# Kernel optimization log

Hardware: AMD Instinct MI355X
Metric: run time of the kernel (lower is better)

Reference implementation:

```python
import jax, jax.numpy as jnp
import numpy as np


def _build_skew(coeff, gate, left, right):
    # coeff: [B, r], gate: [B], left/right: [F, r]
    scaled_left = left[None, :, :] * coeff[:, None, :]          # [B, F, r]
    base = jnp.einsum('bfr,gr->bfg', scaled_left, right)         # [B, F, F]
    skew = base - jnp.swapaxes(base, -1, -2)
    return gate[:, None, None] * skew


def setup_inputs() -> dict:
    key = jax.random.key(0)
    ks = jax.random.split(key, 10)
    B, N, F, R = 8, 4096, 512, 16
    return {
        'x': jax.random.normal(ks[0], (B, N, F), dtype=jnp.float32),
        'coeff': jax.random.normal(ks[1], (B, R), dtype=jnp.float32),
        'gate': jax.random.uniform(ks[2], (B,), dtype=jnp.float32),
        'coeff_local': jax.random.normal(ks[3], (B, R), dtype=jnp.float32),
        'gate_local': jax.random.uniform(ks[4], (B,), dtype=jnp.float32),
        'comm_scale': jax.random.uniform(ks[5], (B,), dtype=jnp.float32),
        'left': jax.random.normal(ks[6], (F, R), dtype=jnp.float32) / np.sqrt(F),
        'right': jax.random.normal(ks[7], (F, R), dtype=jnp.float32) / np.sqrt(F),
        'left_local': jax.random.normal(ks[8], (F, R), dtype=jnp.float32) / np.sqrt(F),
        'right_local': jax.random.normal(ks[9], (F, R), dtype=jnp.float32) / np.sqrt(F),
    }


def reference(x, coeff, gate, coeff_local, gate_local, comm_scale,
              left, right, left_local, right_local):
    F_dim = left.shape[0]
    global_skew = _build_skew(coeff, gate, left, right)                  # [B, F, F]
    local_skew = _build_skew(coeff_local, gate_local, left_local, right_local)
    omega = 0.5 * (global_skew + local_skew)
    commutator = local_skew @ global_skew - global_skew @ local_skew
    omega = omega + comm_scale[:, None, None] * (commutator / 12.0)
    eye = jnp.eye(F_dim, dtype=jnp.float32)[None, :, :]
    # Cayley transform: (I - 0.5*Omega)^{-1} (I + 0.5*Omega)
    transform = jnp.linalg.solve(eye - 0.5 * omega, eye + 0.5 * omega)   # [B, F, F]
    mixed = jnp.einsum('bnd,bdh->bnh', x, transform)
    return mixed.astype(x.dtype)
```

## Files before the change

kernel.cpp:

```cpp
#include <hip/hip_runtime.h>

#define B_ 8
#define N_ 4096
#define F_ 512

typedef __attribute__((ext_vector_type(8))) short bf16x8;
typedef __attribute__((ext_vector_type(4))) float f32x4;

__device__ __forceinline__ float Sval(const float* l, const float* r,
                                      const float* ll, const float* rl,
                                      int h, int e) {
    const int m = e >> 4, c = e & 15;
    const float* p = (m == 0) ? l : (m == 1) ? r : (m == 2) ? ll : rl;
    return p[h * 16 + c];
}

__device__ __forceinline__ float qval(const float* coeff, const float* coeff_l,
                                      int b, int j) {
    if (j < 16) return 1.f;
    if (j < 32) return coeff[b * 16 + (j - 16)];
    if (j < 48) return 1.f;
    return coeff_l[b * 16 + (j - 48)];
}

__device__ __forceinline__ float lane_bcast(float v, int lane) {
    return __int_as_float(__builtin_amdgcn_readlane(__float_as_int(v), lane));
}

__device__ __forceinline__ unsigned short bf16_rn(float x) {
    unsigned u = __float_as_uint(x);
    unsigned r = u + 0x7FFFu + ((u >> 16) & 1u);
    return (unsigned short)(r >> 16);
}

__device__ __forceinline__ void bf16_split(float x, short& hi, short& lo) {
    const unsigned short h = bf16_rn(x);
    const float hf = __uint_as_float(((unsigned)h) << 16);
    const unsigned short s = bf16_rn(x - hf);
    hi = (short)h; lo = (short)s;
}

__global__ __launch_bounds__(256) void k_prep(const float* l, const float* r,
                                              const float* ll, const float* rl,
                                              float* GS, unsigned short* Sf) {
    __shared__ float red[4][64];
    const int i = blockIdx.x;
    const int t = threadIdx.x;
    const int j = t & 63, seg = t >> 6;

    {
        const int ht = i >> 1, eh = i & 1;
        for (int idx = t; idx < 512; idx += 256) {
            const int lx = idx >> 3, ii = idx & 7;
            const int h = ht * 16 + (lx & 15);
            const int e = eh * 32 + ((lx >> 4) & 3) * 8 + ii;
            short hh, ss;
            bf16_split(Sval(l, r, ll, rl, h, e), hh, ss);
            Sf[(i * 2 + 0) * 512 + idx] = (unsigned short)hh;
            Sf[(i * 2 + 1) * 512 + idx] = (unsigned short)ss;
        }
    }

    float acc = 0.f;
    const int h0 = seg * 128;
    for (int h = h0; h < h0 + 128; ++h)
        acc += Sval(l, r, ll, rl, h, i) * Sval(l, r, ll, rl, h, j);
    red[seg][j] = acc;
    __syncthreads();
    if (t < 64) GS[i * 64 + t] = red[0][t] + red[1][t] + red[2][t] + red[3][t];
}

#define DO64(M, K) \
    M(0, K) M(1, K) M(2, K) M(3, K) M(4, K) M(5, K) M(6, K) M(7, K) \
    M(8, K) M(9, K) M(10, K) M(11, K) M(12, K) M(13, K) M(14, K) M(15, K) \
    M(16, K) M(17, K) M(18, K) M(19, K) M(20, K) M(21, K) M(22, K) M(23, K) \
    M(24, K) M(25, K) M(26, K) M(27, K) M(28, K) M(29, K) M(30, K) M(31, K) \
    M(32, K) M(33, K) M(34, K) M(35, K) M(36, K) M(37, K) M(38, K) M(39, K) \
    M(40, K) M(41, K) M(42, K) M(43, K) M(44, K) M(45, K) M(46, K) M(47, K) \
    M(48, K) M(49, K) M(50, K) M(51, K) M(52, K) M(53, K) M(54, K) M(55, K) \
    M(56, K) M(57, K) M(58, K) M(59, K) M(60, K) M(61, K) M(62, K) M(63, K)

#define GJ_LOAD(RR, K) a[RR] = MsL[(RR) * 64 + t];
#define GJ_STORE(RR, K) KsL[(RR) * 64 + t] = a[RR];
#define GJ_UPD(RR, K) \
    if ((RR) != (K)) { \
        const float f = lane_bcast(a[RR], (K)); \
        a[RR] = ((t == (K)) ? 0.f : a[RR]) - f * a[K]; \
    }
#define GJ_STEP(K) { \
    const float dk = lane_bcast(a[K], (K)); \
    const float pinv = 1.0f / dk; \
    a[K] = (t == (K)) ? pinv : a[K] * pinv; \
    DO64(GJ_UPD, K) \
}

__global__ __launch_bounds__(256, 1) void k_solve(const float* coeff, const float* gate,
                                                  const float* coeff_l, const float* gate_l,
                                                  const float* comm, const float* GS,
                                                  float* Eout) {
    __shared__ float smem[16384];
    float* CPs = smem;
    float* GST = smem + 4096;
    float* MsL = smem + 8192;
    float* KsL = smem + 12288;
    float* ABs = MsL;
    float* u1s = KsL;
    float* u2s = KsL + 32;

    const int b = blockIdx.x, t = threadIdx.x;
    const int tx = t & 15, ty = t >> 4;
    const float g = gate[b], gl = gate_l[b];
    const float cs = comm[b] / 12.0f;

    if (t < 32) {
        u1s[t] = (t < 16) ? g * coeff[b * 16 + t] : -g;
        u2s[t] = (t < 16) ? gl * coeff_l[b * 16 + t] : -gl;
    }
    for (int idx = t; idx < 4096; idx += 256) {
        const int i = idx & 63, e = idx >> 6;
        GST[idx] = -0.5f * qval(coeff, coeff_l, b, i) * GS[(i ^ 16) * 64 + e];
    }
    __syncthreads();

    for (int idx = t; idx < 2048; idx += 256) {
        const int which = idx >> 10;
        const int i = (idx >> 5) & 31, j = idx & 31;
        float val;
        if (which == 0) {
            const int v2i = (i < 16) ? 48 + i : 16 + i;
            const float v2sc = (i < 16) ? 1.f : coeff_l[b * 16 + (i - 16)];
            val = v2sc * u1s[j] * GS[v2i * 64 + j];
        } else {
            const int v1i = (i < 16) ? 16 + i : i - 16;
            const float v1sc = (i < 16) ? 1.f : coeff[b * 16 + (i - 16)];
            val = v1sc * u2s[j] * GS[v1i * 64 + 32 + j];
        }
        ABs[idx] = val;
    }
    __syncthreads();

    for (int idx = t; idx < 4096; idx += 256) {
        const int e = idx >> 6, j = idx & 63;
        float val = 0.f;
        if (j < 32) {
            if (e == j) val += 0.5f * u1s[j];
            if (e >= 32) val += cs * u2s[e - 32] * ABs[(e - 32) * 32 + j];
        } else {
            const int jp = j - 32;
            if (e == 32 + jp) val += 0.5f * u2s[jp];
            if (e < 32) val -= cs * u1s[e] * ABs[1024 + e * 32 + jp];
        }
        CPs[idx] = val;
    }
    __syncthreads();

    {
        const int i0 = ty * 4, m0 = tx * 4;
        float acc[4][4];
#pragma unroll
        for (int i = 0; i < 4; ++i)
#pragma unroll
            for (int j = 0; j < 4; ++j) acc[i][j] = 0.f;
        for (int e = 0; e < 64; ++e) {
            const float4 av = *reinterpret_cast<const float4*>(&GST[e * 64 + i0]);
            const float4 bv = *reinterpret_cast<const float4*>(&CPs[e * 64 + m0]);
            const float a[4] = {av.x, av.y, av.z, av.w};
            const float bb[4] = {bv.x, bv.y, bv.z, bv.w};
#pragma unroll
            for (int i = 0; i < 4; ++i)
#pragma unroll
                for (int j = 0; j < 4; ++j) acc[i][j] += a[i] * bb[j];
        }
        __syncthreads();
#pragma unroll
        for (int i = 0; i < 4; ++i)
#pragma unroll
            for (int j = 0; j < 4; ++j)
                MsL[(i0 + i) * 64 + m0 + j] =
                    acc[i][j] + (((i0 + i) == (m0 + j)) ? 1.f : 0.f);
    }
    __syncthreads();

    if (t < 64) {
        float a[64];
        DO64(GJ_LOAD, 0)
        GJ_STEP(0) GJ_STEP(1) GJ_STEP(2) GJ_STEP(3)
        GJ_STEP(4) GJ_STEP(5) GJ_STEP(6) GJ_STEP(7)
        GJ_STEP(8) GJ_STEP(9) GJ_STEP(10) GJ_STEP(11)
        GJ_STEP(12) GJ_STEP(13) GJ_STEP(14) GJ_STEP(15)
        GJ_STEP(16) GJ_STEP(17) GJ_STEP(18) GJ_STEP(19)
        GJ_STEP(20) GJ_STEP(21) GJ_STEP(22) GJ_STEP(23)
        GJ_STEP(24) GJ_STEP(25) GJ_STEP(26) GJ_STEP(27)
        GJ_STEP(28) GJ_STEP(29) GJ_STEP(30) GJ_STEP(31)
        GJ_STEP(32) GJ_STEP(33) GJ_STEP(34) GJ_STEP(35)
        GJ_STEP(36) GJ_STEP(37) GJ_STEP(38) GJ_STEP(39)
        GJ_STEP(40) GJ_STEP(41) GJ_STEP(42) GJ_STEP(43)
        GJ_STEP(44) GJ_STEP(45) GJ_STEP(46) GJ_STEP(47)
        GJ_STEP(48) GJ_STEP(49) GJ_STEP(50) GJ_STEP(51)
        GJ_STEP(52) GJ_STEP(53) GJ_STEP(54) GJ_STEP(55)
        GJ_STEP(56) GJ_STEP(57) GJ_STEP(58) GJ_STEP(59)
        GJ_STEP(60) GJ_STEP(61) GJ_STEP(62) GJ_STEP(63)
        DO64(GJ_STORE, 0)
    }
    __syncthreads();

    {
        const int i0 = ty * 4, j0 = tx * 4;
        float accd[4][4], acca[4][4];
#pragma unroll
        for (int i = 0; i < 4; ++i)
#pragma unroll
            for (int j = 0; j < 4; ++j) { accd[i][j] = 0.f; acca[i][j] = 0.f; }
        for (int q = 0; q < 64; ++q) {
            const float4 bv = *reinterpret_cast<const float4*>(&KsL[q * 64 + j0]);
            const float bb[4] = {bv.x, bv.y, bv.z, bv.w};
            float ad[4], aa[4];
#pragma unroll
            for (int i = 0; i < 4; ++i) {
                ad[i] = CPs[(i0 + i) * 64 + q];
                aa[i] = MsL[(i0 + i) * 64 + q];
            }
#pragma unroll
            for (int i = 0; i < 4; ++i)
#pragma unroll
                for (int j = 0; j < 4; ++j) {
                    accd[i][j] += ad[i] * bb[j];
                    acca[i][j] += aa[i] * bb[j];
                }
        }
        __syncthreads();
#pragma unroll
        for (int i = 0; i < 4; ++i)
#pragma unroll
            for (int j = 0; j < 4; ++j) {
                GST[(i0 + i) * 64 + j0 + j] = accd[i][j];
                CPs[(i0 + i) * 64 + j0 + j] = acca[i][j];
            }
    }
    __syncthreads();

    {
        const int e0 = ty * 4, c0 = tx * 4;
        float acc[4][4];
#pragma unroll
        for (int i = 0; i < 4; ++i)
#pragma unroll
            for (int j = 0; j < 4; ++j) acc[i][j] = 0.f;
        for (int q = 0; q < 64; ++q) {
            const float4 bv = *reinterpret_cast<const float4*>(&CPs[q * 64 + c0]);
            const float bb[4] = {bv.x, bv.y, bv.z, bv.w};
            float a[4];
#pragma unroll
            for (int i = 0; i < 4; ++i) a[i] = GST[(e0 + i) * 64 + q];
#pragma unroll
            for (int i = 0; i < 4; ++i)
#pragma unroll
                for (int j = 0; j < 4; ++j) acc[i][j] += a[i] * bb[j];
        }
        float qv[4];
#pragma unroll
        for (int j = 0; j < 4; ++j) qv[j] = qval(coeff, coeff_l, b, c0 + j);
#pragma unroll
        for (int i = 0; i < 4; ++i) {
            float4 o;
            o.x = qv[0] * (2.f * GST[(e0 + i) * 64 + c0 + 0] - acc[i][0]);
            o.y = qv[1] * (2.f * GST[(e0 + i) * 64 + c0 + 1] - acc[i][1]);
            o.z = qv[2] * (2.f * GST[(e0 + i) * 64 + c0 + 2] - acc[i][2]);
            o.w = qv[3] * (2.f * GST[(e0 + i) * 64 + c0 + 3] - acc[i][3]);
            *reinterpret_cast<float4*>(&Eout[b * 4096 + (e0 + i) * 64 + (c0 ^ 16)]) = o;
        }
    }
}

__global__ __launch_bounds__(256) void k_se(const float* l, const float* r,
                                            const float* ll, const float* rl,
                                            const float* Ein, unsigned short* SEf) {
    __shared__ float Es[4096];
    __shared__ float Ss[64 * 66];
    __shared__ float SEs[64 * 65];
    const int b = blockIdx.y, hc = blockIdx.x, t = threadIdx.x;
    for (int idx = t; idx < 4096; idx += 256) {
        Es[idx] = Ein[b * 4096 + idx];
        const int hl_ = idx >> 6, e = idx & 63;
        Ss[hl_ * 66 + e] = Sval(l, r, ll, rl, hc * 64 + hl_, e);
    }
    __syncthreads();

    const int h = t >> 2;
    const int mg = (t & 3) * 16;
    float acc[16];
#pragma unroll
    for (int q = 0; q < 16; ++q) acc[q] = 0.f;
#pragma unroll 4
    for (int e = 0; e < 64; ++e) {
        const float s = Ss[h * 66 + e];
        const float* Er = Es + e * 64 + mg;
#pragma unroll
        for (int q = 0; q < 16; ++q) acc[q] += s * Er[q];
    }
#pragma unroll
    for (int q = 0; q < 16; ++q) SEs[h * 65 + mg + q] = acc[q];
    __syncthreads();

    unsigned short* outp = SEf + (size_t)b * 65536 + hc * 8192;
#pragma unroll
    for (int it = 0; it < 4; ++it) {
        const int widx0 = it * 2048 + t * 8;
        const int fl = widx0 >> 10;
        const int hl = (widx0 >> 9) & 1;
        const int lx = (widx0 >> 3) & 63;
        const int m = (fl & 3) * 16 + (lx & 15);
        const int hb = (fl >> 2) * 32 + ((lx >> 4) & 3) * 8;
        unsigned short wv[8];
#pragma unroll
        for (int i = 0; i < 8; ++i) {
            short hh, ss;
            bf16_split(SEs[(hb + i) * 65 + m], hh, ss);
            wv[i] = hl ? (unsigned short)ss : (unsigned short)hh;
        }
        uint4 pk;
        pk.x = (unsigned)wv[0] | ((unsigned)wv[1] << 16);
        pk.y = (unsigned)wv[2] | ((unsigned)wv[3] << 16);
        pk.z = (unsigned)wv[4] | ((unsigned)wv[5] << 16);
        pk.w = (unsigned)wv[6] | ((unsigned)wv[7] << 16);
        *reinterpret_cast<uint4*>(outp + widx0) = pk;
    }
}

__global__ __launch_bounds__(256, 4) void k_mix(const float* x,
                                                const unsigned short* SEf,
                                                const unsigned short* Sf,
                                                float* out) {
    __shared__ float Zs[32 * 68];
    const int b = blockIdx.y;
    const int r0 = blockIdx.x * 32;
    const int t = threadIdx.x;
    const int w = t >> 6;
    const int l = t & 63;
    const int lm = l & 15;
    const int lk = (l >> 4) * 8;
    const int rw = w & 1, cw = w >> 1;
    const float* xb = x + (size_t)b * N_ * F_;
    float* outb = out + (size_t)b * N_ * F_;
    const unsigned short* sef = SEf + (size_t)b * 65536;

    f32x4 ahh0 = {0.f, 0.f, 0.f, 0.f}, alh0 = ahh0, ahl0 = ahh0;
    f32x4 ahh1 = ahh0, alh1 = ahh0, ahl1 = ahh0;
    const int arow = r0 + 16 * rw + lm;
    const float* xrow = xb + (size_t)arow * F_;
#pragma unroll 2
    for (int kk = 0; kk < 16; ++kk) {
        const int k0 = kk * 32 + lk;
        const float4 xa = *reinterpret_cast<const float4*>(xrow + k0);
        const float4 xc = *reinterpret_cast<const float4*>(xrow + k0 + 4);
        const float xs[8] = {xa.x, xa.y, xa.z, xa.w, xc.x, xc.y, xc.z, xc.w};
        bf16x8 ah, al;
#pragma unroll
        for (int i = 0; i < 8; ++i) {
            short hh, ss;
            bf16_split(xs[i], hh, ss);
            ah[i] = hh; al[i] = ss;
        }
        const int o0 = (kk * 4 + 2 * cw) * 1024 + l * 8;
        const bf16x8 bh0 = *reinterpret_cast<const bf16x8*>(sef + o0);
        const bf16x8 bl0 = *reinterpret_cast<const bf16x8*>(sef + o0 + 512);
        const bf16x8 bh1 = *reinterpret_cast<const bf16x8*>(sef + o0 + 1024);
        const bf16x8 bl1 = *reinterpret_cast<const bf16x8*>(sef + o0 + 1536);
        ahh0 = __builtin_amdgcn_mfma_f32_16x16x32_bf16(ah, bh0, ahh0, 0, 0, 0);
        alh0 = __builtin_amdgcn_mfma_f32_16x16x32_bf16(al, bh0, alh0, 0, 0, 0);
        ahl0 = __builtin_amdgcn_mfma_f32_16x16x32_bf16(ah, bl0, ahl0, 0, 0, 0);
        ahh1 = __builtin_amdgcn_mfma_f32_16x16x32_bf16(ah, bh1, ahh1, 0, 0, 0);
        alh1 = __builtin_amdgcn_mfma_f32_16x16x32_bf16(al, bh1, alh1, 0, 0, 0);
        ahl1 = __builtin_amdgcn_mfma_f32_16x16x32_bf16(ah, bl1, ahl1, 0, 0, 0);
    }
#pragma unroll
    for (int r = 0; r < 4; ++r) {
        const int zr = (16 * rw + (l >> 4) * 4 + r) * 68 + 32 * cw;
        Zs[zr + lm] = ahh0[r] + alh0[r] + ahl0[r];
        Zs[zr + 16 + lm] = ahh1[r] + alh1[r] + ahl1[r];
    }
    __syncthreads();

    bf16x8 zh0, zl0, zh1, zl1;
    {
        const float* zrow = &Zs[(16 * rw + lm) * 68];
#pragma unroll
        for (int i = 0; i < 8; ++i) {
            short hh, ss;
            bf16_split(zrow[lk + i], hh, ss);
            zh0[i] = hh; zl0[i] = ss;
            bf16_split(zrow[32 + lk + i], hh, ss);
            zh1[i] = hh; zl1[i] = ss;
        }
    }
    const int orow0 = r0 + 16 * rw + (l >> 4) * 4;
#pragma unroll 2
    for (int j2 = 0; j2 < 16; ++j2) {
        const int ht = cw * 16 + j2;
        const int h0 = ht * 16 + lm;
        f32x4 ca = {0.f, 0.f, 0.f, 0.f};
        f32x4 cb;
#pragma unroll
        for (int r = 0; r < 4; ++r) cb[r] = xb[(size_t)(orow0 + r) * F_ + h0];
        const int fb = ht * 2048 + l * 8;
        const bf16x8 bh0 = *reinterpret_cast<const bf16x8*>(Sf + fb);
        const bf16x8 bl0 = *reinterpret_cast<const bf16x8*>(Sf + fb + 512);
        const bf16x8 bh1 = *reinterpret_cast<const bf16x8*>(Sf + fb + 1024);
        const bf16x8 bl1 = *reinterpret_cast<const bf16x8*>(Sf + fb + 1536);
        ca = __builtin_amdgcn_mfma_f32_16x16x32_bf16(zh0, bh0, ca, 0, 0, 0);
        ca = __builtin_amdgcn_mfma_f32_16x16x32_bf16(zl0, bh0, ca, 0, 0, 0);
        ca = __builtin_amdgcn_mfma_f32_16x16x32_bf16(zh0, bl0, ca, 0, 0, 0);
        cb = __builtin_amdgcn_mfma_f32_16x16x32_bf16(zh1, bh1, cb, 0, 0, 0);
        cb = __builtin_amdgcn_mfma_f32_16x16x32_bf16(zl1, bh1, cb, 0, 0, 0);
        cb = __builtin_amdgcn_mfma_f32_16x16x32_bf16(zh1, bl1, cb, 0, 0, 0);
#pragma unroll
        for (int r = 0; r < 4; ++r)
            outb[(size_t)(orow0 + r) * F_ + h0] = ca[r] + cb[r];
    }
}

extern "C" void kernel_launch(void* const* d_in, const int* in_sizes, int n_in,
                              void* d_out, int out_size, void* d_ws, size_t ws_size,
                              hipStream_t stream) {
    (void)in_sizes; (void)n_in; (void)out_size; (void)ws_size;
    const float* x       = (const float*)d_in[0];
    const float* coeff   = (const float*)d_in[1];
    const float* gate    = (const float*)d_in[2];
    const float* coeff_l = (const float*)d_in[3];
    const float* gate_l  = (const float*)d_in[4];
    const float* comm    = (const float*)d_in[5];
    const float* l       = (const float*)d_in[6];
    const float* r       = (const float*)d_in[7];
    const float* ll      = (const float*)d_in[8];
    const float* rl      = (const float*)d_in[9];

    char* wsb = (char*)d_ws;
    float* GS = (float*)(wsb);
    float* E  = (float*)(wsb + 16384);
    unsigned short* SEf = (unsigned short*)(wsb + 147456);
    unsigned short* Sf  = (unsigned short*)(wsb + 1196032);
    float* out = (float*)d_out;

    k_prep<<<dim3(64), dim3(256), 0, stream>>>(l, r, ll, rl, GS, Sf);
    k_solve<<<dim3(8), dim3(256), 0, stream>>>(coeff, gate, coeff_l, gate_l, comm, GS, E);
    k_se<<<dim3(8, 8), dim3(256), 0, stream>>>(l, r, ll, rl, E, SEf);
    k_mix<<<dim3(128, 8), dim3(256), 0, stream>>>(x, SEf, Sf, out);
}
```

Baseline: 123.7 us.

## Split small-matrix solve kernel into pre, Gauss-Jordan inverse, and post kernels

The fused k_solve kernel is split into three launches. k_pre builds M and CP and writes them to workspace. k_inv runs the 64x64 register-resident Gauss-Jordan inverse in a 64-thread block, and k_post does the trailing matmuls. This separates the register-heavy inverse from the 256-thread shared-memory matmul phases, which may improve register allocation and remove idle threads during the inverse. The cost is two extra launches and global-memory round trips for M, CP and K on a tiny 8-block serial path.

```diff
diff --git a/kernel.cpp b/kernel.cpp
--- a/kernel.cpp
+++ b/kernel.cpp
@@ -70,42 +70,14 @@
     if (t < 64) GS[i * 64 + t] = red[0][t] + red[1][t] + red[2][t] + red[3][t];
 }
 
-#define DO64(M, K) \
-    M(0, K) M(1, K) M(2, K) M(3, K) M(4, K) M(5, K) M(6, K) M(7, K) \
-    M(8, K) M(9, K) M(10, K) M(11, K) M(12, K) M(13, K) M(14, K) M(15, K) \
-    M(16, K) M(17, K) M(18, K) M(19, K) M(20, K) M(21, K) M(22, K) M(23, K) \
-    M(24, K) M(25, K) M(26, K) M(27, K) M(28, K) M(29, K) M(30, K) M(31, K) \
-    M(32, K) M(33, K) M(34, K) M(35, K) M(36, K) M(37, K) M(38, K) M(39, K) \
-    M(40, K) M(41, K) M(42, K) M(43, K) M(44, K) M(45, K) M(46, K) M(47, K) \
-    M(48, K) M(49, K) M(50, K) M(51, K) M(52, K) M(53, K) M(54, K) M(55, K) \
-    M(56, K) M(57, K) M(58, K) M(59, K) M(60, K) M(61, K) M(62, K) M(63, K)
-
-#define GJ_LOAD(RR, K) a[RR] = MsL[(RR) * 64 + t];
-#define GJ_STORE(RR, K) KsL[(RR) * 64 + t] = a[RR];
-#define GJ_UPD(RR, K) \
-    if ((RR) != (K)) { \
-        const float f = lane_bcast(a[RR], (K)); \
-        a[RR] = ((t == (K)) ? 0.f : a[RR]) - f * a[K]; \
-    }
-#define GJ_STEP(K) { \
-    const float dk = lane_bcast(a[K], (K)); \
-    const float pinv = 1.0f / dk; \
-    a[K] = (t == (K)) ? pinv : a[K] * pinv; \
-    DO64(GJ_UPD, K) \
-}
-
-__global__ __launch_bounds__(256, 1) void k_solve(const float* coeff, const float* gate,
-                                                  const float* coeff_l, const float* gate_l,
-                                                  const float* comm, const float* GS,
-                                                  float* Eout) {
-    __shared__ float smem[16384];
-    float* CPs = smem;
-    float* GST = smem + 4096;
-    float* MsL = smem + 8192;
-    float* KsL = smem + 12288;
-    float* ABs = MsL;
-    float* u1s = KsL;
-    float* u2s = KsL + 32;
+__global__ __launch_bounds__(256) void k_pre(const float* coeff, const float* gate,
+                                             const float* coeff_l, const float* gate_l,
+                                             const float* comm, const float* GS,
+                                             float* Mws, float* CPws) {
+    __shared__ float GST[4096];
+    __shared__ float CPs[4096];
+    __shared__ float ABs[2048];
+    __shared__ float u1s[32], u2s[32];
 
     const int b = blockIdx.x, t = threadIdx.x;
     const int tx = t & 15, ty = t >> 4;
@@ -151,6 +123,7 @@
             if (e < 32) val -= cs * u1s[e] * ABs[1024 + e * 32 + jp];
         }
         CPs[idx] = val;
+        CPws[b * 4096 + idx] = val;
     }
     __syncthreads();
 
@@ -171,36 +144,77 @@
 #pragma unroll
                 for (int j = 0; j < 4; ++j) acc[i][j] += a[i] * bb[j];
         }
-        __syncthreads();
-#pragma unroll
-        for (int i = 0; i < 4; ++i)
-#pragma unroll
-            for (int j = 0; j < 4; ++j)
-                MsL[(i0 + i) * 64 + m0 + j] =
-                    acc[i][j] + (((i0 + i) == (m0 + j)) ? 1.f : 0.f);
-    }
-    __syncthreads();
-
-    if (t < 64) {
-        float a[64];
-        DO64(GJ_LOAD, 0)
-        GJ_STEP(0) GJ_STEP(1) GJ_STEP(2) GJ_STEP(3)
-        GJ_STEP(4) GJ_STEP(5) GJ_STEP(6) GJ_STEP(7)
-        GJ_STEP(8) GJ_STEP(9) GJ_STEP(10) GJ_STEP(11)
-        GJ_STEP(12) GJ_STEP(13) GJ_STEP(14) GJ_STEP(15)
-        GJ_STEP(16) GJ_STEP(17) GJ_STEP(18) GJ_STEP(19)
-        GJ_STEP(20) GJ_STEP(21) GJ_STEP(22) GJ_STEP(23)
-        GJ_STEP(24) GJ_STEP(25) GJ_STEP(26) GJ_STEP(27)
-        GJ_STEP(28) GJ_STEP(29) GJ_STEP(30) GJ_STEP(31)
-        GJ_STEP(32) GJ_STEP(33) GJ_STEP(34) GJ_STEP(35)
-        GJ_STEP(36) GJ_STEP(37) GJ_STEP(38) GJ_STEP(39)
-        GJ_STEP(40) GJ_STEP(41) GJ_STEP(42) GJ_STEP(43)
-        GJ_STEP(44) GJ_STEP(45) GJ_STEP(46) GJ_STEP(47)
-        GJ_STEP(48) GJ_STEP(49) GJ_STEP(50) GJ_STEP(51)
-        GJ_STEP(52) GJ_STEP(53) GJ_STEP(54) GJ_STEP(55)
-        GJ_STEP(56) GJ_STEP(57) GJ_STEP(58) GJ_STEP(59)
-        GJ_STEP(60) GJ_STEP(61) GJ_STEP(62) GJ_STEP(63)
-        DO64(GJ_STORE, 0)
+#pragma unroll
+        for (int i = 0; i < 4; ++i) {
+            float4 o;
+            o.x = acc[i][0] + (((i0 + i) == (m0 + 0)) ? 1.f : 0.f);
+            o.y = acc[i][1] + (((i0 + i) == (m0 + 1)) ? 1.f : 0.f);
+            o.z = acc[i][2] + (((i0 + i) == (m0 + 2)) ? 1.f : 0.f);
+            o.w = acc[i][3] + (((i0 + i) == (m0 + 3)) ? 1.f : 0.f);
+            *reinterpret_cast<float4*>(&Mws[b * 4096 + (i0 + i) * 64 + m0]) = o;
+        }
+    }
+}
+
+#define DO64(M, K) \
+    M(0, K) M(1, K) M(2, K) M(3, K) M(4, K) M(5, K) M(6, K) M(7, K) \
+    M(8, K) M(9, K) M(10, K) M(11, K) M(12, K) M(13, K) M(14, K) M(15, K) \
+    M(16, K) M(17, K) M(18, K) M(19, K) M(20, K) M(21, K) M(22, K) M(23, K) \
+    M(24, K) M(25, K) M(26, K) M(27, K) M(28, K) M(29, K) M(30, K) M(31, K) \
+    M(32, K) M(33, K) M(34, K) M(35, K) M(36, K) M(37, K) M(38, K) M(39, K) \
+    M(40, K) M(41, K) M(42, K) M(43, K) M(44, K) M(45, K) M(46, K) M(47, K) \
+    M(48, K) M(49, K) M(50, K) M(51, K) M(52, K) M(53, K) M(54, K) M(55, K) \
+    M(56, K) M(57, K) M(58, K) M(59, K) M(60, K) M(61, K) M(62, K) M(63, K)
+
+#define GJ_LOAD(RR, K) a[RR] = Mws[base + (RR)*64 + t];
+#define GJ_STORE(RR, K) Kws[base + (RR)*64 + t] = a[RR];
+#define GJ_UPD(RR, K) \
+    if ((RR) != (K)) { \
+        const float f = lane_bcast(a[RR], (K)); \
+        a[RR] = ((t == (K)) ? 0.f : a[RR]) - f * a[K]; \
+    }
+#define GJ_STEP(K) { \
+    const float dk = lane_bcast(a[K], (K)); \
+    const float pinv = 1.0f / dk; \
+    a[K] = (t == (K)) ? pinv : a[K] * pinv; \
+    DO64(GJ_UPD, K) \
+}
+
+__global__ __launch_bounds__(64, 1) void k_inv(const float* Mws, float* Kws) {
+    const int b = blockIdx.x, t = threadIdx.x;
+    const int base = b * 4096;
+    float a[64];
+    DO64(GJ_LOAD, 0)
+    GJ_STEP(0) GJ_STEP(1) GJ_STEP(2) GJ_STEP(3)
+    GJ_STEP(4) GJ_STEP(5) GJ_STEP(6) GJ_STEP(7)
+    GJ_STEP(8) GJ_STEP(9) GJ_STEP(10) GJ_STEP(11)
+    GJ_STEP(12) GJ_STEP(13) GJ_STEP(14) GJ_STEP(15)
+    GJ_STEP(16) GJ_STEP(17) GJ_STEP(18) GJ_STEP(19)
+    GJ_STEP(20) GJ_STEP(21) GJ_STEP(22) GJ_STEP(23)
+    GJ_STEP(24) GJ_STEP(25) GJ_STEP(26) GJ_STEP(27)
+    GJ_STEP(28) GJ_STEP(29) GJ_STEP(30) GJ_STEP(31)
+    GJ_STEP(32) GJ_STEP(33) GJ_STEP(34) GJ_STEP(35)
+    GJ_STEP(36) GJ_STEP(37) GJ_STEP(38) GJ_STEP(39)
+    GJ_STEP(40) GJ_STEP(41) GJ_STEP(42) GJ_STEP(43)
+    GJ_STEP(44) GJ_STEP(45) GJ_STEP(46) GJ_STEP(47)
+    GJ_STEP(48) GJ_STEP(49) GJ_STEP(50) GJ_STEP(51)
+    GJ_STEP(52) GJ_STEP(53) GJ_STEP(54) GJ_STEP(55)
+    GJ_STEP(56) GJ_STEP(57) GJ_STEP(58) GJ_STEP(59)
+    GJ_STEP(60) GJ_STEP(61) GJ_STEP(62) GJ_STEP(63)
+    DO64(GJ_STORE, 0)
+}
+
+__global__ __launch_bounds__(256) void k_post(const float* coeff, const float* coeff_l,
+                                              const float* Mws, const float* CPws,
+                                              const float* Kws, float* Eout) {
+    __shared__ float Ms[4096], CPs[4096], Ks[4096], Tds[4096], Tas[4096];
+    const int b = blockIdx.x, t = threadIdx.x;
+    const int tx = t & 15, ty = t >> 4;
+
+    for (int idx = t; idx < 4096; idx += 256) {
+        Ms[idx] = Mws[b * 4096 + idx];
+        CPs[idx] = CPws[b * 4096 + idx];
+        Ks[idx] = Kws[b * 4096 + idx];
     }
     __syncthreads();
 
@@ -212,13 +226,13 @@
 #pragma unroll
             for (int j = 0; j < 4; ++j) { accd[i][j] = 0.f; acca[i][j] = 0.f; }
         for (int q = 0; q < 64; ++q) {
-            const float4 bv = *reinterpret_cast<const float4*>(&KsL[q * 64 + j0]);
+            const float4 bv = *reinterpret_cast<const float4*>(&Ks[q * 64 + j0]);
             const float bb[4] = {bv.x, bv.y, bv.z, bv.w};
             float ad[4], aa[4];
 #pragma unroll
             for (int i = 0; i < 4; ++i) {
                 ad[i] = CPs[(i0 + i) * 64 + q];
-                aa[i] = MsL[(i0 + i) * 64 + q];
+                aa[i] = Ms[(i0 + i) * 64 + q];
             }
 #pragma unroll
             for (int i = 0; i < 4; ++i)
@@ -228,13 +242,12 @@
                     acca[i][j] += aa[i] * bb[j];
                 }
         }
-        __syncthreads();
 #pragma unroll
         for (int i = 0; i < 4; ++i)
 #pragma unroll
             for (int j = 0; j < 4; ++j) {
-                GST[(i0 + i) * 64 + j0 + j] = accd[i][j];
-                CPs[(i0 + i) * 64 + j0 + j] = acca[i][j];
+                Tds[(i0 + i) * 64 + j0 + j] = accd[i][j];
+                Tas[(i0 + i) * 64 + j0 + j] = acca[i][j];
             }
     }
     __syncthreads();
@@ -247,11 +260,11 @@
 #pragma unroll
             for (int j = 0; j < 4; ++j) acc[i][j] = 0.f;
         for (int q = 0; q < 64; ++q) {
-            const float4 bv = *reinterpret_cast<const float4*>(&CPs[q * 64 + c0]);
+            const float4 bv = *reinterpret_cast<const float4*>(&Tas[q * 64 + c0]);
             const float bb[4] = {bv.x, bv.y, bv.z, bv.w};
             float a[4];
 #pragma unroll
-            for (int i = 0; i < 4; ++i) a[i] = GST[(e0 + i) * 64 + q];
+            for (int i = 0; i < 4; ++i) a[i] = Tds[(e0 + i) * 64 + q];
 #pragma unroll
             for (int i = 0; i < 4; ++i)
 #pragma unroll
@@ -263,10 +276,10 @@
 #pragma unroll
         for (int i = 0; i < 4; ++i) {
             float4 o;
-            o.x = qv[0] * (2.f * GST[(e0 + i) * 64 + c0 + 0] - acc[i][0]);
-            o.y = qv[1] * (2.f * GST[(e0 + i) * 64 + c0 + 1] - acc[i][1]);
-            o.z = qv[2] * (2.f * GST[(e0 + i) * 64 + c0 + 2] - acc[i][2]);
-            o.w = qv[3] * (2.f * GST[(e0 + i) * 64 + c0 + 3] - acc[i][3]);
+            o.x = qv[0] * (2.f * Tds[(e0 + i) * 64 + c0 + 0] - acc[i][0]);
+            o.y = qv[1] * (2.f * Tds[(e0 + i) * 64 + c0 + 1] - acc[i][1]);
+            o.z = qv[2] * (2.f * Tds[(e0 + i) * 64 + c0 + 2] - acc[i][2]);
+            o.w = qv[3] * (2.f * Tds[(e0 + i) * 64 + c0 + 3] - acc[i][3]);
             *reinterpret_cast<float4*>(&Eout[b * 4096 + (e0 + i) * 64 + (c0 ^ 16)]) = o;
         }
     }
@@ -435,14 +448,20 @@
     const float* rl      = (const float*)d_in[9];
 
     char* wsb = (char*)d_ws;
-    float* GS = (float*)(wsb);
-    float* E  = (float*)(wsb + 16384);
+    float* GS   = (float*)(wsb);
+    float* E    = (float*)(wsb + 16384);
     unsigned short* SEf = (unsigned short*)(wsb + 147456);
     unsigned short* Sf  = (unsigned short*)(wsb + 1196032);
+    float* Mws  = (float*)(wsb + 1327104);
+    float* CPws = (float*)(wsb + 1458176);
+    float* Kws  = (float*)(wsb + 1589248);
     float* out = (float*)d_out;
 
     k_prep<<<dim3(64), dim3(256), 0, stream>>>(l, r, ll, rl, GS, Sf);
-    k_solve<<<dim3(8), dim3(256), 0, stream>>>(coeff, gate, coeff_l, gate_l, comm, GS, E);
+    k_pre<<<dim3(8), dim3(256), 0, stream>>>(coeff, gate, coeff_l, gate_l, comm, GS,
+                                             Mws, CPws);
+    k_inv<<<dim3(8), dim3(64), 0, stream>>>(Mws, Kws);
+    k_post<<<dim3(8), dim3(256), 0, stream>>>(coeff, coeff_l, Mws, CPws, Kws, E);
     k_se<<<dim3(8, 8), dim3(256), 0, stream>>>(l, r, ll, rl, E, SEf);
     k_mix<<<dim3(128, 8), dim3(256), 0, stream>>>(x, SEf, Sf, out);
 }
```

Measured after the change: 134.7 us. 8.9% more time.
